# Kernel optimization log

Measured on AMD Instinct MI355X. Metric: run time of the kernel, lower is better.

## Reference

```python
import jax, jax.numpy as jnp
import numpy as np

B, L, K = 4096, 4096, 10


def _sparsemax(z):
    # z: [..., n]; Martins & Astudillo sparsemax along last dim
    n = z.shape[-1]
    zs = -jnp.sort(-z, axis=-1)                      # descending
    cum = jnp.cumsum(zs, axis=-1)
    r = jnp.arange(1, n + 1, dtype=z.dtype)
    support = (1.0 + r * zs) > cum                   # [..., n]
    ksel = jnp.sum(support, axis=-1, keepdims=True)  # support size
    tau = (jnp.take_along_axis(cum, ksel - 1, axis=-1) - 1.0) / ksel.astype(z.dtype)
    return jnp.maximum(z - tau, 0.0)


def _topk_bitvectors(logits, k):
    # k highest-scoring binary vectors z in {0,1}^L under <z, logits>
    # (faithful to the CPU batched_topk: detached logits)
    lg = jax.lax.stop_gradient(logits)
    b, latent = lg.shape
    base = (lg > 0).astype(lg.dtype)                 # argmax config [B, L]
    costs = jnp.abs(lg)                              # flip costs
    neg_small, pos = jax.lax.top_k(-costs, k)        # k smallest costs + positions
    c_small = -neg_small                             # [B, k]
    m = 1 << k                                       # 2^k candidate flip subsets
    bits = ((jnp.arange(m)[:, None] >> jnp.arange(k)[None, :]) & 1).astype(lg.dtype)  # [2^k, k]
    sums = jnp.einsum('mk,bk->bm', bits, c_small)    # total flip cost per subset
    _, best = jax.lax.top_k(-sums, k)                # k cheapest subsets [B, k]
    flips = bits[best]                               # [B, k, k] which small-cost bits to flip
    base_at = jnp.take_along_axis(base, pos, axis=1) # base bit value at flip positions [B, k]
    delta = flips * (1.0 - 2.0 * base_at[:, None, :])  # +1 or -1 where flipped
    bv = jnp.broadcast_to(base[:, None, :], (b, k, latent))
    bidx = jnp.arange(b)[:, None, None]
    cidx = jnp.arange(k)[None, :, None]
    jpos = pos[:, None, :]                           # [B, 1, k]
    bv = bv.at[bidx, cidx, jpos].add(delta)          # scatter flips -> [B, k, L]
    return bv


def reference(logits, k):
    bv = _topk_bitvectors(logits, k)                         # [B, k, L]
    scores = jnp.einsum('bkj,bj->bk', bv, logits)            # [B, k]
    distr = _sparsemax(scores)                               # [B, k]
    p = distr.reshape(-1)
    safe_p = jnp.where(p > 0, p, 1.0)
    entropy = -jnp.sum(jnp.where(p > 0, p * jnp.log(safe_p), 0.0))
    batch_size = logits.shape[0]
    return bv, distr, entropy / batch_size


def setup_inputs() -> dict:
    key = jax.random.key(0)
    logits = jax.random.normal(key, (B, L), dtype=jnp.float32)
    return {"logits": logits, "k": K}
```

## Files before the change

kernel.cpp:

```cpp
#include <hip/hip_runtime.h>
#include <stdint.h>

#define NB   4096
#define LDIM 4096
#define KK   10
#define TPB  256
#define CAP  1024

typedef float fx4 __attribute__((ext_vector_type(4)));

__device__ __forceinline__ unsigned long long wave_min_u64(unsigned long long v) {
#pragma unroll
    for (int off = 1; off < 64; off <<= 1) {
        const unsigned long long o = __shfl_xor(v, off, 64);
        if (o < v) v = o;
    }
    return v;
}

__global__ __launch_bounds__(TPB) void select_rows(
    const float* __restrict__ logits,
    float* __restrict__ distr,
    float* __restrict__ entp,
    unsigned* __restrict__ meta,
    unsigned* __restrict__ basebits)
{
    __shared__ float s_wsum[4];
    __shared__ int   s_pos[KK];
    __shared__ int   s_sign[KK];
    __shared__ int   s_bestm[KK];
    __shared__ int   s_cnt;
    __shared__ unsigned s_base[128];
    __shared__ unsigned long long s_cand[CAP];

    const int b    = blockIdx.x;
    const int t    = threadIdx.x;
    const int lane = t & 63;
    const int wv   = t >> 6;
    const float* __restrict__ row = logits + (size_t)b * LDIM;

    float vals[16];
#pragma unroll
    for (int q = 0; q < 4; q++) {
        const float4 f = *(const float4*)(row + (q << 10) + (t << 2));
        vals[q*4+0] = f.x; vals[q*4+1] = f.y; vals[q*4+2] = f.z; vals[q*4+3] = f.w;
    }

    float s0 = 0.f;
#pragma unroll
    for (int i = 0; i < 16; i++) s0 += vals[i] > 0.f ? vals[i] : 0.f;
#pragma unroll
    for (int off = 1; off < 64; off <<= 1) s0 += __shfl_xor(s0, off, 64);
    if (lane == 0) s_wsum[wv] = s0;

    if (t < 128) s_base[t] = 0u;
    __syncthreads();
#pragma unroll
    for (int q = 0; q < 4; q++) {
        unsigned nib = 0u;
#pragma unroll
        for (int e = 0; e < 4; e++)
            nib |= (vals[q*4+e] > 0.f ? 1u : 0u) << e;
        atomicOr(&s_base[(q << 5) + (t >> 3)], nib << (4 * (t & 7)));
    }

    float T = 0.02f;
    int cnt = 0;
    for (int attempt = 0; attempt < 15; attempt++) {
        if (t == 0) s_cnt = 0;
        __syncthreads();
#pragma unroll
        for (int i = 0; i < 16; i++) {
            const float v    = vals[i];
            const float cost = fabsf(v);
            if (cost < T) {
                const int idx = ((i >> 2) << 10) + (t << 2) + (i & 3);
                const unsigned long long pk =
                    ((unsigned long long)__float_as_uint(cost) << 32)
                    | (unsigned)((idx << 1) | (v > 0.f ? 1 : 0));
                const int p = atomicAdd(&s_cnt, 1);
                if (p < CAP) s_cand[p] = pk;
            }
        }
        __syncthreads();
        cnt = s_cnt;
        if (cnt >= KK && cnt <= CAP) break;
        T = (cnt < KK) ? T * 4.0f : T * 0.25f;
        __syncthreads();
    }

    if (t < 128) basebits[b * 128 + t] = s_base[t];

    if (wv != 0) return;

    const float S0 = (s_wsum[0] + s_wsum[1]) + (s_wsum[2] + s_wsum[3]);
    float csm[KK];
    unsigned long long prev = 0ull;

    if (cnt >= KK && cnt <= CAP) {
        const int nc = cnt;
#pragma unroll
        for (int c = 0; c < KK; c++) {
            unsigned long long best = ~0ull;
            for (int p = lane; p < nc; p += 64) {
                const unsigned long long pk = s_cand[p];
                if ((c == 0 || pk > prev) && pk < best) best = pk;
            }
            best = wave_min_u64(best);
            prev = best;
            csm[c] = __uint_as_float((unsigned)(best >> 32));
            if (lane == 0) {
                const unsigned lo = (unsigned)best;
                s_pos[c]  = (int)(lo >> 1);
                s_sign[c] = (int)(lo & 1u);
            }
        }
    } else {
#pragma unroll
        for (int c = 0; c < KK; c++) {
            unsigned long long best = ~0ull;
            for (int p = lane; p < LDIM; p += 64) {
                const float v    = row[p];
                const float cost = fabsf(v);
                const unsigned long long pk =
                    ((unsigned long long)__float_as_uint(cost) << 32)
                    | (unsigned)((p << 1) | (v > 0.f ? 1 : 0));
                if ((c == 0 || pk > prev) && pk < best) best = pk;
            }
            best = wave_min_u64(best);
            prev = best;
            csm[c] = __uint_as_float((unsigned)(best >> 32));
            if (lane == 0) {
                const unsigned lo = (unsigned)best;
                s_pos[c]  = (int)(lo >> 1);
                s_sign[c] = (int)(lo & 1u);
            }
        }
    }

    float sums[16];
#pragma unroll
    for (int i = 0; i < 16; i++) {
        const int m = (lane << 4) | i;
        float acc = 0.f;
#pragma unroll
        for (int j = 0; j < KK; j++) acc += (m & (1 << j)) ? csm[j] : 0.f;
        sums[i] = acc;
    }

    float zc[KK];
    unsigned long long prev2 = 0ull;
#pragma unroll
    for (int c = 0; c < KK; c++) {
        unsigned long long best = ~0ull;
#pragma unroll
        for (int i = 0; i < 16; i++) {
            const unsigned long long pk =
                ((unsigned long long)__float_as_uint(sums[i]) << 32)
                | (unsigned)((lane << 4) | i);
            if ((c == 0 || pk > prev2) && pk < best) best = pk;
        }
        best = wave_min_u64(best);
        prev2 = best;
        zc[c] = S0 - __uint_as_float((unsigned)(best >> 32));
        if (lane == 0) s_bestm[c] = (int)((unsigned)best & 1023u);
    }

    if (lane == 0) {
        float acc = 0.f; int ks = 0;
#pragma unroll
        for (int r = 1; r <= KK; r++) {
            acc += zc[r-1];
            if (1.f + (float)r * zc[r-1] > acc) ks++;
        }
        float acc2 = 0.f;
#pragma unroll
        for (int r = 0; r < KK; r++) if (r < ks) acc2 += zc[r];
        const float tau = (acc2 - 1.f) / (float)ks;
        float entl = 0.f;
        float* drow = distr + b * KK;
#pragma unroll
        for (int c = 0; c < KK; c++) {
            float p = zc[c] - tau;
            p = p > 0.f ? p : 0.f;
            drow[c] = p;
            if (p > 0.f) entl -= p * logf(p);
        }
        entp[b] = entl;

        unsigned* mrow = meta + b * KK;
#pragma unroll
        for (int s = 0; s < KK; s++) {
            unsigned fm = 0u;
#pragma unroll
            for (int c = 0; c < KK; c++)
                fm |= (((unsigned)s_bestm[c] >> s) & 1u) << c;
            mrow[s] = (unsigned)s_pos[s] | (fm << 12) | ((unsigned)s_sign[s] << 22);
        }
    }
}

__global__ __launch_bounds__(TPB) void bv_writer(
    const unsigned* __restrict__ basebits,
    const unsigned* __restrict__ meta,
    float* __restrict__ bv)
{
    __shared__ unsigned s_base[128];
    __shared__ unsigned s_m[KK];
    const int c = blockIdx.x;
    const int b = blockIdx.y;
    const int t = threadIdx.x;

    if (t < 128) s_base[t] = basebits[b * 128 + t];
    else if (t < 128 + KK) s_m[t - 128] = meta[b * KK + (t - 128)];
    __syncthreads();

    unsigned bits = 0u;
#pragma unroll
    for (int u = 0; u < 4; u++)
        bits |= ((s_base[(u << 5) + (t >> 3)] >> (4 * (t & 7))) & 0xFu) << (4 * u);

#pragma unroll
    for (int s = 0; s < KK; s++) {
        const unsigned m   = s_m[s];
        const int      pos = (int)(m & 0xFFFu);
        const unsigned flp = (m >> (12 + c)) & 1u;
        if (((pos & 1023) >> 2) == t)
            bits ^= flp << (4 * (pos >> 10) + (pos & 3));
    }

    float* out = bv + ((size_t)b * KK + c) * LDIM + (t << 2);
#pragma unroll
    for (int u = 0; u < 4; u++) {
        fx4 v;
        v.x = (bits >> (4*u + 0)) & 1u ? 1.f : 0.f;
        v.y = (bits >> (4*u + 1)) & 1u ? 1.f : 0.f;
        v.z = (bits >> (4*u + 2)) & 1u ? 1.f : 0.f;
        v.w = (bits >> (4*u + 3)) & 1u ? 1.f : 0.f;
        *(fx4*)(out + (u << 10)) = v;
    }
}

__global__ __launch_bounds__(256) void ent_reduce(
    const float* __restrict__ ws, float* __restrict__ ent)
{
    __shared__ float sw[4];
    const int t = threadIdx.x, lane = t & 63, wv = t >> 6;
    float s = 0.f;
    for (int i = t; i < NB; i += 256) s += ws[i];
#pragma unroll
    for (int off = 1; off < 64; off <<= 1) s += __shfl_xor(s, off, 64);
    if (lane == 0) sw[wv] = s;
    __syncthreads();
    if (t == 0) *ent = (sw[0] + sw[1] + sw[2] + sw[3]) * (1.0f / (float)NB);
}

__global__ __launch_bounds__(TPB) void topk_sparsemax_fused(
    const float* __restrict__ logits,
    float* __restrict__ bv,
    float* __restrict__ distr,
    float* __restrict__ ent)
{
    __shared__ float s_wsum[4];
    __shared__ int   s_pos[KK];
    __shared__ int   s_sign[KK];
    __shared__ int   s_bestm[KK];
    __shared__ int   s_cnt;
    __shared__ unsigned long long s_cand[CAP];

    const int b    = blockIdx.x;
    const int t    = threadIdx.x;
    const int lane = t & 63;
    const int wv   = t >> 6;
    const float* __restrict__ row = logits + (size_t)b * LDIM;

    float vals[16];
#pragma unroll
    for (int q = 0; q < 4; q++) {
        const float4 f = *(const float4*)(row + (q << 10) + (t << 2));
        vals[q*4+0] = f.x; vals[q*4+1] = f.y; vals[q*4+2] = f.z; vals[q*4+3] = f.w;
    }

    float s0 = 0.f;
#pragma unroll
    for (int i = 0; i < 16; i++) s0 += vals[i] > 0.f ? vals[i] : 0.f;
#pragma unroll
    for (int off = 1; off < 64; off <<= 1) s0 += __shfl_xor(s0, off, 64);
    if (lane == 0) s_wsum[wv] = s0;

    float T = 0.02f;
    int cnt = 0;
    for (int attempt = 0; attempt < 15; attempt++) {
        if (t == 0) s_cnt = 0;
        __syncthreads();
#pragma unroll
        for (int i = 0; i < 16; i++) {
            const float v    = vals[i];
            const float cost = fabsf(v);
            if (cost < T) {
                const int idx = ((i >> 2) << 10) + (t << 2) + (i & 3);
                const unsigned long long pk =
                    ((unsigned long long)__float_as_uint(cost) << 32)
                    | (unsigned)((idx << 1) | (v > 0.f ? 1 : 0));
                const int p = atomicAdd(&s_cnt, 1);
                if (p < CAP) s_cand[p] = pk;
            }
        }
        __syncthreads();
        cnt = s_cnt;
        if (cnt >= KK && cnt <= CAP) break;
        T = (cnt < KK) ? T * 4.0f : T * 0.25f;
        __syncthreads();
    }

    if (wv == 0) {
        const float S0 = (s_wsum[0] + s_wsum[1]) + (s_wsum[2] + s_wsum[3]);
        float csm[KK];
        unsigned long long prev = 0ull;
        if (cnt >= KK && cnt <= CAP) {
            const int nc = cnt;
#pragma unroll
            for (int c = 0; c < KK; c++) {
                unsigned long long best = ~0ull;
                for (int p = lane; p < nc; p += 64) {
                    const unsigned long long pk = s_cand[p];
                    if ((c == 0 || pk > prev) && pk < best) best = pk;
                }
                best = wave_min_u64(best);
                prev = best;
                csm[c] = __uint_as_float((unsigned)(best >> 32));
                if (lane == 0) {
                    const unsigned lo = (unsigned)best;
                    s_pos[c]  = (int)(lo >> 1);
                    s_sign[c] = (int)(lo & 1u);
                }
            }
        } else {
#pragma unroll
            for (int c = 0; c < KK; c++) {
                unsigned long long best = ~0ull;
                for (int p = lane; p < LDIM; p += 64) {
                    const float v    = row[p];
                    const float cost = fabsf(v);
                    const unsigned long long pk =
                        ((unsigned long long)__float_as_uint(cost) << 32)
                        | (unsigned)((p << 1) | (v > 0.f ? 1 : 0));
                    if ((c == 0 || pk > prev) && pk < best) best = pk;
                }
                best = wave_min_u64(best);
                prev = best;
                csm[c] = __uint_as_float((unsigned)(best >> 32));
                if (lane == 0) {
                    const unsigned lo = (unsigned)best;
                    s_pos[c]  = (int)(lo >> 1);
                    s_sign[c] = (int)(lo & 1u);
                }
            }
        }
        float sums[16];
#pragma unroll
        for (int i = 0; i < 16; i++) {
            const int m = (lane << 4) | i;
            float acc = 0.f;
#pragma unroll
            for (int j = 0; j < KK; j++) acc += (m & (1 << j)) ? csm[j] : 0.f;
            sums[i] = acc;
        }
        float zc[KK];
        unsigned long long prev2 = 0ull;
#pragma unroll
        for (int c = 0; c < KK; c++) {
            unsigned long long best = ~0ull;
#pragma unroll
            for (int i = 0; i < 16; i++) {
                const unsigned long long pk =
                    ((unsigned long long)__float_as_uint(sums[i]) << 32)
                    | (unsigned)((lane << 4) | i);
                if ((c == 0 || pk > prev2) && pk < best) best = pk;
            }
            best = wave_min_u64(best);
            prev2 = best;
            zc[c] = S0 - __uint_as_float((unsigned)(best >> 32));
            if (lane == 0) s_bestm[c] = (int)((unsigned)best & 1023u);
        }
        if (lane == 0) {
            float acc = 0.f; int ks = 0;
#pragma unroll
            for (int r = 1; r <= KK; r++) {
                acc += zc[r-1];
                if (1.f + (float)r * zc[r-1] > acc) ks++;
            }
            float acc2 = 0.f;
#pragma unroll
            for (int r = 0; r < KK; r++) if (r < ks) acc2 += zc[r];
            const float tau = (acc2 - 1.f) / (float)ks;
            float entl = 0.f;
            float* drow = distr + b * KK;
#pragma unroll
            for (int c = 0; c < KK; c++) {
                float p = zc[c] - tau;
                p = p > 0.f ? p : 0.f;
                drow[c] = p;
                if (p > 0.f) entl -= p * logf(p);
            }
            atomicAdd(ent, entl * (1.0f / (float)NB));
        }
    }

    __syncthreads();

    unsigned fm[KK];
#pragma unroll
    for (int j = 0; j < KK; j++) {
        unsigned m = 0u;
#pragma unroll
        for (int c = 0; c < KK; c++)
            m |= (((unsigned)s_bestm[c] >> j) & 1u) << c;
        fm[j] = m;
    }
    int posr[KK], sgnr[KK];
#pragma unroll
    for (int j = 0; j < KK; j++) { posr[j] = s_pos[j]; sgnr[j] = s_sign[j]; }

    unsigned rowflip[16]; float flipval[16]; float basef[16];
#pragma unroll
    for (int i = 0; i < 16; i++) {
        const int col = ((i >> 2) << 10) + (t << 2) + (i & 3);
        unsigned rfm = 0u; float fvv = 0.f;
#pragma unroll
        for (int j = 0; j < KK; j++) {
            if (posr[j] == col) { rfm = fm[j]; fvv = sgnr[j] ? 0.f : 1.f; }
        }
        rowflip[i] = rfm; flipval[i] = fvv;
        basef[i]   = vals[i] > 0.f ? 1.f : 0.f;
    }

    float* out0 = bv + (size_t)b * (KK * LDIM);
#pragma unroll
    for (int c = 0; c < KK; c++) {
        float* orow = out0 + c * LDIM + (t << 2);
#pragma unroll
        for (int q = 0; q < 4; q++) {
            fx4 v;
            v.x = ((rowflip[q*4+0] >> c) & 1u) ? flipval[q*4+0] : basef[q*4+0];
            v.y = ((rowflip[q*4+1] >> c) & 1u) ? flipval[q*4+1] : basef[q*4+1];
            v.z = ((rowflip[q*4+2] >> c) & 1u) ? flipval[q*4+2] : basef[q*4+2];
            v.w = ((rowflip[q*4+3] >> c) & 1u) ? flipval[q*4+3] : basef[q*4+3];
            __builtin_nontemporal_store(v, (fx4*)(orow + (q << 10)));
        }
    }
}

extern "C" void kernel_launch(void* const* d_in, const int* in_sizes, int n_in,
                              void* d_out, int out_size, void* d_ws, size_t ws_size,
                              hipStream_t stream)
{
    const float* logits = (const float*)d_in[0];
    float* out   = (float*)d_out;
    float* bv    = out;
    float* distr = out + (size_t)NB * KK * LDIM;
    float* ent   = distr + (size_t)NB * KK;

    const size_t need = (size_t)NB * sizeof(float)
                      + (size_t)NB * KK * sizeof(unsigned)
                      + (size_t)NB * 128 * sizeof(unsigned);
    if (ws_size >= need) {
        float*    entp = (float*)d_ws;
        unsigned* meta = (unsigned*)((float*)d_ws + NB);
        unsigned* bbit = meta + (size_t)NB * KK;
        select_rows<<<dim3(NB), dim3(TPB), 0, stream>>>(logits, distr, entp, meta, bbit);
        bv_writer <<<dim3(KK, NB), dim3(TPB), 0, stream>>>(bbit, meta, bv);
        ent_reduce<<<dim3(1), dim3(256), 0, stream>>>(entp, ent);
    } else {
        (void)hipMemsetAsync(ent, 0, sizeof(float), stream);
        topk_sparsemax_fused<<<dim3(NB), dim3(TPB), 0, stream>>>(logits, bv, distr, ent);
    }
}
```

Before: 716.6 us.

## Materialize per-candidate bit rows in select kernel; expand with grid-stride streaming kernel

select_rows now applies the flips itself and writes a full packed bit row per candidate (K×128 words per batch row) to the workspace, in place of base bits plus per-flip metadata. The writer kernel becomes a flat grid-stride expander over a fixed 2048-block grid that turns each nibble into a float4 and writes it with a nontemporal store. The aim is to simplify the dominant 671 MB output write into a uniform streaming pattern with fewer blocks and less per-block setup. In exchange there is an extra ~21 MB of workspace traffic and a barrier that the other three waves in select_rows now wait on.

```diff
diff --git a/kernel.cpp b/kernel.cpp
--- a/kernel.cpp
+++ b/kernel.cpp
@@ -7,6 +7,9 @@
 #define TPB  256
 #define CAP  1024
 
+#define WPR  (KK * 128)
+#define TOT4 ((size_t)NB * KK * LDIM / 4)
+
 typedef float fx4 __attribute__((ext_vector_type(4)));
 
 __device__ __forceinline__ unsigned long long wave_min_u64(unsigned long long v) {
@@ -22,8 +25,7 @@
     const float* __restrict__ logits,
     float* __restrict__ distr,
     float* __restrict__ entp,
-    unsigned* __restrict__ meta,
-    unsigned* __restrict__ basebits)
+    unsigned* __restrict__ fullbits)
 {
     __shared__ float s_wsum[4];
     __shared__ int   s_pos[KK];
@@ -89,155 +91,137 @@
         __syncthreads();
     }
 
-    if (t < 128) basebits[b * 128 + t] = s_base[t];
-
-    if (wv != 0) return;
-
-    const float S0 = (s_wsum[0] + s_wsum[1]) + (s_wsum[2] + s_wsum[3]);
-    float csm[KK];
-    unsigned long long prev = 0ull;
-
-    if (cnt >= KK && cnt <= CAP) {
-        const int nc = cnt;
+    if (wv == 0) {
+        const float S0 = (s_wsum[0] + s_wsum[1]) + (s_wsum[2] + s_wsum[3]);
+        float csm[KK];
+        unsigned long long prev = 0ull;
+
+        if (cnt >= KK && cnt <= CAP) {
+            const int nc = cnt;
+#pragma unroll
+            for (int c = 0; c < KK; c++) {
+                unsigned long long best = ~0ull;
+                for (int p = lane; p < nc; p += 64) {
+                    const unsigned long long pk = s_cand[p];
+                    if ((c == 0 || pk > prev) && pk < best) best = pk;
+                }
+                best = wave_min_u64(best);
+                prev = best;
+                csm[c] = __uint_as_float((unsigned)(best >> 32));
+                if (lane == 0) {
+                    const unsigned lo = (unsigned)best;
+                    s_pos[c]  = (int)(lo >> 1);
+                    s_sign[c] = (int)(lo & 1u);
+                }
+            }
+        } else {
+#pragma unroll
+            for (int c = 0; c < KK; c++) {
+                unsigned long long best = ~0ull;
+                for (int p = lane; p < LDIM; p += 64) {
+                    const float v    = row[p];
+                    const float cost = fabsf(v);
+                    const unsigned long long pk =
+                        ((unsigned long long)__float_as_uint(cost) << 32)
+                        | (unsigned)((p << 1) | (v > 0.f ? 1 : 0));
+                    if ((c == 0 || pk > prev) && pk < best) best = pk;
+                }
+                best = wave_min_u64(best);
+                prev = best;
+                csm[c] = __uint_as_float((unsigned)(best >> 32));
+                if (lane == 0) {
+                    const unsigned lo = (unsigned)best;
+                    s_pos[c]  = (int)(lo >> 1);
+                    s_sign[c] = (int)(lo & 1u);
+                }
+            }
+        }
+
+        float sums[16];
+#pragma unroll
+        for (int i = 0; i < 16; i++) {
+            const int m = (lane << 4) | i;
+            float acc = 0.f;
+#pragma unroll
+            for (int j = 0; j < KK; j++) acc += (m & (1 << j)) ? csm[j] : 0.f;
+            sums[i] = acc;
+        }
+
+        float zc[KK];
+        unsigned long long prev2 = 0ull;
 #pragma unroll
         for (int c = 0; c < KK; c++) {
             unsigned long long best = ~0ull;
-            for (int p = lane; p < nc; p += 64) {
-                const unsigned long long pk = s_cand[p];
-                if ((c == 0 || pk > prev) && pk < best) best = pk;
+#pragma unroll
+            for (int i = 0; i < 16; i++) {
+                const unsigned long long pk =
+                    ((unsigned long long)__float_as_uint(sums[i]) << 32)
+                    | (unsigned)((lane << 4) | i);
+                if ((c == 0 || pk > prev2) && pk < best) best = pk;
             }
             best = wave_min_u64(best);
-            prev = best;
-            csm[c] = __uint_as_float((unsigned)(best >> 32));
-            if (lane == 0) {
-                const unsigned lo = (unsigned)best;
-                s_pos[c]  = (int)(lo >> 1);
-                s_sign[c] = (int)(lo & 1u);
-            }
-        }
-    } else {
-#pragma unroll
-        for (int c = 0; c < KK; c++) {
-            unsigned long long best = ~0ull;
-            for (int p = lane; p < LDIM; p += 64) {
-                const float v    = row[p];
-                const float cost = fabsf(v);
-                const unsigned long long pk =
-                    ((unsigned long long)__float_as_uint(cost) << 32)
-                    | (unsigned)((p << 1) | (v > 0.f ? 1 : 0));
-                if ((c == 0 || pk > prev) && pk < best) best = pk;
-            }
-            best = wave_min_u64(best);
-            prev = best;
-            csm[c] = __uint_as_float((unsigned)(best >> 32));
-            if (lane == 0) {
-                const unsigned lo = (unsigned)best;
-                s_pos[c]  = (int)(lo >> 1);
-                s_sign[c] = (int)(lo & 1u);
-            }
-        }
-    }
-
-    float sums[16];
-#pragma unroll
-    for (int i = 0; i < 16; i++) {
-        const int m = (lane << 4) | i;
-        float acc = 0.f;
-#pragma unroll
-        for (int j = 0; j < KK; j++) acc += (m & (1 << j)) ? csm[j] : 0.f;
-        sums[i] = acc;
-    }
-
-    float zc[KK];
-    unsigned long long prev2 = 0ull;
-#pragma unroll
-    for (int c = 0; c < KK; c++) {
-        unsigned long long best = ~0ull;
-#pragma unroll
-        for (int i = 0; i < 16; i++) {
-            const unsigned long long pk =
-                ((unsigned long long)__float_as_uint(sums[i]) << 32)
-                | (unsigned)((lane << 4) | i);
-            if ((c == 0 || pk > prev2) && pk < best) best = pk;
-        }
-        best = wave_min_u64(best);
-        prev2 = best;
-        zc[c] = S0 - __uint_as_float((unsigned)(best >> 32));
-        if (lane == 0) s_bestm[c] = (int)((unsigned)best & 1023u);
-    }
-
-    if (lane == 0) {
-        float acc = 0.f; int ks = 0;
-#pragma unroll
-        for (int r = 1; r <= KK; r++) {
-            acc += zc[r-1];
-            if (1.f + (float)r * zc[r-1] > acc) ks++;
-        }
-        float acc2 = 0.f;
-#pragma unroll
-        for (int r = 0; r < KK; r++) if (r < ks) acc2 += zc[r];
-        const float tau = (acc2 - 1.f) / (float)ks;
-        float entl = 0.f;
-        float* drow = distr + b * KK;
-#pragma unroll
-        for (int c = 0; c < KK; c++) {
-            float p = zc[c] - tau;
-            p = p > 0.f ? p : 0.f;
-            drow[c] = p;
-            if (p > 0.f) entl -= p * logf(p);
-        }
-        entp[b] = entl;
-
-        unsigned* mrow = meta + b * KK;
+            prev2 = best;
+            zc[c] = S0 - __uint_as_float((unsigned)(best >> 32));
+            if (lane == 0) s_bestm[c] = (int)((unsigned)best & 1023u);
+        }
+
+        if (lane == 0) {
+            float acc = 0.f; int ks = 0;
+#pragma unroll
+            for (int r = 1; r <= KK; r++) {
+                acc += zc[r-1];
+                if (1.f + (float)r * zc[r-1] > acc) ks++;
+            }
+            float acc2 = 0.f;
+#pragma unroll
+            for (int r = 0; r < KK; r++) if (r < ks) acc2 += zc[r];
+            const float tau = (acc2 - 1.f) / (float)ks;
+            float entl = 0.f;
+            float* drow = distr + b * KK;
+#pragma unroll
+            for (int c = 0; c < KK; c++) {
+                float p = zc[c] - tau;
+                p = p > 0.f ? p : 0.f;
+                drow[c] = p;
+                if (p > 0.f) entl -= p * logf(p);
+            }
+            entp[b] = entl;
+        }
+    }
+
+    __syncthreads();
+    unsigned* frow = fullbits + (size_t)b * WPR;
+#pragma unroll
+    for (int r = 0; r < WPR / TPB; r++) {
+        const int i = t + r * TPB;
+        const int c = i >> 7;
+        const int w = i & 127;
+        unsigned word = s_base[w];
 #pragma unroll
         for (int s = 0; s < KK; s++) {
-            unsigned fm = 0u;
-#pragma unroll
-            for (int c = 0; c < KK; c++)
-                fm |= (((unsigned)s_bestm[c] >> s) & 1u) << c;
-            mrow[s] = (unsigned)s_pos[s] | (fm << 12) | ((unsigned)s_sign[s] << 22);
-        }
-    }
-}
-
-__global__ __launch_bounds__(TPB) void bv_writer(
-    const unsigned* __restrict__ basebits,
-    const unsigned* __restrict__ meta,
+            const int ps = s_pos[s];
+            const unsigned hit = (unsigned)((ps >> 5) == w) & ((unsigned)(s_bestm[c] >> s) & 1u);
+            word ^= hit << (ps & 31);
+        }
+        frow[i] = word;
+    }
+}
+
+#define EXP_BLOCKS 2048
+__global__ __launch_bounds__(TPB) void bv_expand(
+    const unsigned* __restrict__ fullbits,
     float* __restrict__ bv)
 {
-    __shared__ unsigned s_base[128];
-    __shared__ unsigned s_m[KK];
-    const int c = blockIdx.x;
-    const int b = blockIdx.y;
-    const int t = threadIdx.x;
-
-    if (t < 128) s_base[t] = basebits[b * 128 + t];
-    else if (t < 128 + KK) s_m[t - 128] = meta[b * KK + (t - 128)];
-    __syncthreads();
-
-    unsigned bits = 0u;
-#pragma unroll
-    for (int u = 0; u < 4; u++)
-        bits |= ((s_base[(u << 5) + (t >> 3)] >> (4 * (t & 7))) & 0xFu) << (4 * u);
-
-#pragma unroll
-    for (int s = 0; s < KK; s++) {
-        const unsigned m   = s_m[s];
-        const int      pos = (int)(m & 0xFFFu);
-        const unsigned flp = (m >> (12 + c)) & 1u;
-        if (((pos & 1023) >> 2) == t)
-            bits ^= flp << (4 * (pos >> 10) + (pos & 3));
-    }
-
-    float* out = bv + ((size_t)b * KK + c) * LDIM + (t << 2);
-#pragma unroll
-    for (int u = 0; u < 4; u++) {
+    const size_t stride = (size_t)EXP_BLOCKS * TPB;
+    for (size_t f = (size_t)blockIdx.x * TPB + threadIdx.x; f < TOT4; f += stride) {
+        const unsigned word = fullbits[f >> 3];
+        const unsigned nib  = (word >> ((f & 7) << 2)) & 0xFu;
         fx4 v;
-        v.x = (bits >> (4*u + 0)) & 1u ? 1.f : 0.f;
-        v.y = (bits >> (4*u + 1)) & 1u ? 1.f : 0.f;
-        v.z = (bits >> (4*u + 2)) & 1u ? 1.f : 0.f;
-        v.w = (bits >> (4*u + 3)) & 1u ? 1.f : 0.f;
-        *(fx4*)(out + (u << 10)) = v;
+        v.x = (nib & 1u) ? 1.f : 0.f;
+        v.y = (nib & 2u) ? 1.f : 0.f;
+        v.z = (nib & 4u) ? 1.f : 0.f;
+        v.w = (nib & 8u) ? 1.f : 0.f;
+        __builtin_nontemporal_store(v, (fx4*)(bv + (f << 2)));
     }
 }
 
@@ -462,14 +446,12 @@
     float* ent   = distr + (size_t)NB * KK;
 
     const size_t need = (size_t)NB * sizeof(float)
-                      + (size_t)NB * KK * sizeof(unsigned)
-                      + (size_t)NB * 128 * sizeof(unsigned);
+                      + (size_t)NB * WPR * sizeof(unsigned);
     if (ws_size >= need) {
         float*    entp = (float*)d_ws;
-        unsigned* meta = (unsigned*)((float*)d_ws + NB);
-        unsigned* bbit = meta + (size_t)NB * KK;
-        select_rows<<<dim3(NB), dim3(TPB), 0, stream>>>(logits, distr, entp, meta, bbit);
-        bv_writer <<<dim3(KK, NB), dim3(TPB), 0, stream>>>(bbit, meta, bv);
+        unsigned* bits = (unsigned*)((float*)d_ws + NB);
+        select_rows<<<dim3(NB), dim3(TPB), 0, stream>>>(logits, distr, entp, bits);
+        bv_expand <<<dim3(EXP_BLOCKS), dim3(TPB), 0, stream>>>(bits, bv);
         ent_reduce<<<dim3(1), dim3(256), 0, stream>>>(entp, ent);
     } else {
         (void)hipMemsetAsync(ent, 0, sizeof(float), stream);
```

After: 716.1 us. No clear change (-0.1%).
